# Performance work log

Measured on AMD Instinct MI355X. Metric: run time of the kernel, lower is better.

## Reference

```python
import jax, jax.numpy as jnp
import numpy as np

B, CIN, CMID, COUT, H, W = 4, 64, 128, 128, 128, 128
K = 9  # 3x3 taps
EPS = 1e-5


def conv3x3(x, w, b):
    # standard 3x3 conv, stride 1, pad 1, NCHW / OIHW
    y = jax.lax.conv_general_dilated(x, w, (1, 1), ((1, 1), (1, 1)),
                                     dimension_numbers=('NCHW', 'OIHW', 'NCHW'))
    return y + b[None, :, None, None]


def deform_conv3x3(x, offset, w, b):
    # torchvision DeformConv2d semantics (v1, no mask), kernel 3, pad 1, stride 1.
    # offset: [B, 2*K, H, W] with per-tap (dy, dx) pairs.
    Bn, C, Hn, Wn = x.shape
    off = offset.reshape(Bn, K, 2, Hn, Wn)
    off_y, off_x = off[:, :, 0], off[:, :, 1]          # [B,K,H,W]
    ky = (jnp.arange(K) // 3).astype(x.dtype)          # tap row 0..2
    kx = (jnp.arange(K) % 3).astype(x.dtype)           # tap col 0..2
    # sampling positions: p = out_pos - pad + tap + offset
    py = jnp.arange(Hn, dtype=x.dtype)[None, None, :, None] - 1.0 + ky[None, :, None, None] + off_y
    px = jnp.arange(Wn, dtype=x.dtype)[None, None, None, :] - 1.0 + kx[None, :, None, None] + off_x
    y0 = jnp.floor(py); x0 = jnp.floor(px)
    wy1 = py - y0; wx1 = px - x0                       # bilinear fractions
    y0i = y0.astype(jnp.int32); x0i = x0.astype(jnp.int32)
    xf = x.reshape(Bn, C, Hn * Wn)

    def gather(iy, ix):
        valid = ((iy >= 0) & (iy < Hn) & (ix >= 0) & (ix < Wn)).astype(x.dtype)
        idx = jnp.clip(iy, 0, Hn - 1) * Wn + jnp.clip(ix, 0, Wn - 1)  # [B,K,H,W]
        g = jax.vmap(lambda xb, ib: xb[:, ib])(xf, idx)               # [B,C,K,H,W]
        return g, valid

    g00, v00 = gather(y0i, x0i)
    g01, v01 = gather(y0i, x0i + 1)
    g10, v10 = gather(y0i + 1, x0i)
    g11, v11 = gather(y0i + 1, x0i + 1)

    def wmul(g, v, wgt):
        return g * (v * wgt)[:, None]                  # broadcast over channel dim

    sampled = (wmul(g00, v00, (1 - wy1) * (1 - wx1)) +
               wmul(g01, v01, (1 - wy1) * wx1) +
               wmul(g10, v10, wy1 * (1 - wx1)) +
               wmul(g11, v11, wy1 * wx1))              # [B,C,K,H,W]
    out = jnp.einsum('bckhw,ock->bohw', sampled, w.reshape(w.shape[0], C, K))
    return out + b[None, :, None, None]


def batchnorm_relu(x, gamma, beta):
    # training-mode BN: batch statistics over (N,H,W), biased variance
    mean = jnp.mean(x, axis=(0, 2, 3), keepdims=True)
    var = jnp.mean(jnp.square(x - mean), axis=(0, 2, 3), keepdims=True)
    y = (x - mean) * jax.lax.rsqrt(var + EPS)
    return jax.nn.relu(y * gamma[None, :, None, None] + beta[None, :, None, None])


def setup_inputs() -> dict:
    key = jax.random.key(0)
    ks = jax.random.split(key, 13)
    s = 0.05  # small weights keep offsets small / sampling mostly in-bounds
    return {
        'x': jax.random.normal(ks[0], (B, CIN, H, W), jnp.float32),
        'w_off1': jax.random.normal(ks[1], (2 * K, CIN, 3, 3), jnp.float32) * s,
        'b_off1': jnp.zeros((2 * K,), jnp.float32),
        'w1': jax.random.normal(ks[2], (CMID, CIN, 3, 3), jnp.float32) * s,
        'b1': jax.random.normal(ks[3], (CMID,), jnp.float32) * s,
        'g1': jnp.ones((CMID,), jnp.float32),
        'be1': jnp.zeros((CMID,), jnp.float32),
        'w_off2': jax.random.normal(ks[4], (2 * K, CMID, 3, 3), jnp.float32) * s,
        'b_off2': jnp.zeros((2 * K,), jnp.float32),
        'w2': jax.random.normal(ks[5], (COUT, CMID, 3, 3), jnp.float32) * s,
        'b2': jax.random.normal(ks[6], (COUT,), jnp.float32) * s,
        'g2': jnp.ones((COUT,), jnp.float32),
        'be2': jnp.zeros((COUT,), jnp.float32),
    }


def reference(x, w_off1, b_off1, w1, b1, g1, be1, w_off2, b_off2, w2, b2, g2, be2):
    offset1 = conv3x3(x, w_off1, b_off1)
    out = deform_conv3x3(x, offset1, w1, b1)
    out = batchnorm_relu(out, g1, be1)
    offset2 = conv3x3(out, w_off2, b_off2)
    out = deform_conv3x3(out, offset2, w2, b2)
    out = batchnorm_relu(out, g2, be2)
    return out
```

## Files before the change

kernel.cpp:

```cpp
#include <hip/hip_runtime.h>
#include <hip/hip_bf16.h>

#define BB 4
#define H_ 128
#define W_ 128
#define HWP 16384
#define CIN1 64
#define CMID 128
#define KOFF 18

typedef short short8 __attribute__((ext_vector_type(8)));
typedef float floatx4 __attribute__((ext_vector_type(4)));

#define WS_AB   16
#define WS_CVT  288
#define CVT_TOTAL 4447396
#define WS_WF1  4447744
#define WS_WF2  4484608
#define WS_XT   4558336
#define WS_OFF  6655488
#define WS_Y1   7835136
#define WS_Y1T  16223744
#define WS_PART 21600000
#define WS_Y2   WS_Y1

#define R_X     0
#define R_WOFF1 4194304
#define R_BOFF1 4204672
#define R_W1    4204690
#define R_B1    4278418
#define R_G1    4278546
#define R_BE1   4278674
#define R_WOFF2 4278802
#define R_BOFF2 4299538
#define R_W2    4299556
#define R_B2    4447012
#define R_G2    4447140
#define R_BE2   4447268

struct SrcPtrs { const void* p[13]; };

__device__ inline short f2bf(float f) {
    __hip_bfloat16 h = __float2bfloat16(f);
    return *reinterpret_cast<short*>(&h);
}
__device__ inline float bf2f(unsigned short u) {
    return __uint_as_float(((unsigned int)u) << 16);
}
__device__ inline float bfu_lo(unsigned int u) { return __uint_as_float(u << 16); }
__device__ inline float bfu_hi(unsigned int u) { return __uint_as_float(u & 0xFFFF0000u); }
__device__ inline float rl_f(float v, int i) {
    return __int_as_float(__builtin_amdgcn_readlane(__float_as_int(v), i));
}

__global__ void probe_dtype_k(const unsigned int* __restrict__ g1, int* __restrict__ flag) {
    if (threadIdx.x == 0 && blockIdx.x == 0) {
        flag[0] = ((g1[0] & 0xFFFFu) != 0u) ? 1 : 0;
    }
}

__global__ __launch_bounds__(256) void convert_inputs_k(SrcPtrs sp, float* __restrict__ dst,
                                                        const int* __restrict__ flag, int total) {
    int i = blockIdx.x * 256 + threadIdx.x;
    if (i >= total) return;
    constexpr int prefix[13] = {0, R_WOFF1, R_BOFF1, R_W1, R_B1, R_G1, R_BE1,
                                R_WOFF2, R_BOFF2, R_W2, R_B2, R_G2, R_BE2};
    const void* src = sp.p[0];
    int base = 0;
#pragma unroll
    for (int q = 1; q < 13; ++q) {
        if (i >= prefix[q]) { src = sp.p[q]; base = prefix[q]; }
    }
    int local = i - base;
    float v;
    if (flag[0] != 0) {
        v = bf2f(((const unsigned short*)src)[local]);
    } else {
        v = ((const float*)src)[local];
    }
    dst[i] = v;
}

template <int CIN>
__global__ __launch_bounds__(256) void wf_build_k(const float* __restrict__ w, short* __restrict__ wf) {
    constexpr int KSTEPS = CIN * 9 / 32;
    int idx = blockIdx.x * 256 + threadIdx.x;
    int j    = idx & 7;
    int lane = (idx >> 3) & 63;
    int rem  = idx >> 9;
    int ks   = rem % KSTEPS;
    int ct   = rem / KSTEPS;
    int co = ct * 16 + (lane & 15);
    int k  = ks * 32 + (lane >> 4) * 8 + j;
    int ci = k & (CIN - 1);
    int kk = k / CIN;
    wf[idx] = f2bf(w[(co * CIN + ci) * 9 + kk]);
}

__global__ __launch_bounds__(256) void xt_build_k(const float* __restrict__ x, unsigned short* __restrict__ xt) {
    __shared__ __align__(4) short s_t[64 * 66];
    int bi  = blockIdx.x;
    int hw0 = (bi & 255) * 64;
    int b   = bi >> 8;
    int t   = threadIdx.x;
    int hwp = t & 63;
#pragma unroll
    for (int it = 0; it < 16; ++it) {
        int c = it * 4 + (t >> 6);
        float v = x[((long)(b * 64 + c) << 14) + hw0 + hwp];
        s_t[hwp * 66 + c] = f2bf(v);
    }
    __syncthreads();
#pragma unroll
    for (int it = 0; it < 8; ++it) {
        int i  = it * 256 + t;
        int c2 = (i & 31) * 2;
        int hw2 = i >> 5;
        int sv = *(const int*)&s_t[hw2 * 66 + c2];
        *(int*)&xt[((long)((b << 14) + hw0 + hw2)) * 64 + c2] = sv;
    }
}

template <int CIN>
__global__ __launch_bounds__(256) void conv3x3_atomic_k(const float* __restrict__ x,
                                                        const float* __restrict__ w,
                                                        const float* __restrict__ bias,
                                                        float* __restrict__ outp) {
    constexpr int CIQ = CIN / 4;
    int bi = blockIdx.x;
    int h  = bi & 127;
    int b  = (bi >> 7) & 3;
    int q  = bi >> 9;
    int t  = threadIdx.x;
    int wq = t & 127;
    int cg = __builtin_amdgcn_readfirstlane(t >> 7);
    int co0 = cg * 9;
    int ci0 = q * CIQ;

    float acc[9];
#pragma unroll
    for (int j = 0; j < 9; ++j) acc[j] = (q == 0) ? bias[co0 + j] : 0.f;

    const float* xb = x + ((long)(b * CIN + ci0) << 14);
    bool bm = h > 0, bp = h < H_ - 1, bl = wq > 0, br = wq < W_ - 1;
    int rm = (bm ? h - 1 : 0) << 7;
    int rc = h << 7;
    int rp = (bp ? h + 1 : H_ - 1) << 7;

#pragma unroll 2
    for (int ci = 0; ci < CIQ; ++ci) {
        const float* plane = xb + ((long)ci << 14);
        float v0 = plane[rm + wq - 1], v1 = plane[rm + wq], v2 = plane[rm + wq + 1];
        float v3 = plane[rc + wq - 1], v4 = plane[rc + wq], v5 = plane[rc + wq + 1];
        float v6 = plane[rp + wq - 1], v7 = plane[rp + wq], v8 = plane[rp + wq + 1];
        v0 = (bm && bl) ? v0 : 0.f;
        v1 = bm ? v1 : 0.f;
        v2 = (bm && br) ? v2 : 0.f;
        v3 = bl ? v3 : 0.f;
        v5 = br ? v5 : 0.f;
        v6 = (bp && bl) ? v6 : 0.f;
        v7 = bp ? v7 : 0.f;
        v8 = (bp && br) ? v8 : 0.f;
#pragma unroll
        for (int j = 0; j < 9; ++j) {
            const float* wk = w + ((long)(co0 + j) * CIN + ci0 + ci) * 9;
            acc[j] += v0 * wk[0] + v1 * wk[1] + v2 * wk[2]
                    + v3 * wk[3] + v4 * wk[4] + v5 * wk[5]
                    + v6 * wk[6] + v7 * wk[7] + v8 * wk[8];
        }
    }

    long ob = ((long)(b * KOFF + co0) << 14) + (h << 7) + wq;
#pragma unroll
    for (int j = 0; j < 9; ++j) atomicAdd(&outp[ob + ((long)j << 14)], acc[j]);
}

template <int CIN>
__device__ inline void build_table(const float* __restrict__ off, int b, int h, int w0,
                                   int lane, int wv,
                                   int& tpk, float& tw0, float& tw1, float& tw2, float& tw3) {
    tpk = 0; tw0 = tw1 = tw2 = tw3 = 0.f;
    if (lane < 36) {
        int r = wv + 4 * lane;
        int p = r & 15;
        int k = r >> 4;
        int wpix = w0 + p;
        long obase = ((long)(b * KOFF) << 14) + (h << 7) + wpix;
        float oy = off[obase + ((long)(2 * k) << 14)];
        float ox = off[obase + ((long)(2 * k + 1) << 14)];
        float py = (float)(h - 1 + (k / 3)) + oy;
        float px = (float)(wpix - 1 + (k % 3)) + ox;
        float fy = floorf(py), fx = floorf(px);
        float wy = py - fy, wx = px - fx;
        int y0 = (int)fy, x0 = (int)fx;
        int y1 = y0 + 1, x1 = x0 + 1;
        bool vy0 = (y0 >= 0) && (y0 < H_);
        bool vy1 = (y1 >= 0) && (y1 < H_);
        bool vx0 = (x0 >= 0) && (x0 < W_);
        bool vx1 = (x1 >= 0) && (x1 < W_);
        float wy0 = 1.f - wy, wx0 = 1.f - wx;
        tw0 = (vy0 && vx0) ? wy0 * wx0 : 0.f;
        tw1 = (vy0 && vx1) ? wy0 * wx  : 0.f;
        tw2 = (vy1 && vx0) ? wy  * wx0 : 0.f;
        tw3 = (vy1 && vx1) ? wy  * wx  : 0.f;
        int iy0 = min(max(y0, 0), H_ - 1), iy1 = min(max(y1, 0), H_ - 1);
        int ix0 = min(max(x0, 0), W_ - 1), ix1 = min(max(x1, 0), W_ - 1);
        int dx = ix1 - ix0;
        int dy = iy1 - iy0;
        tpk = (iy0 * W_ + ix0) | (dx << 14) | (dy << 15);
    }
}

template <int NB>
__device__ inline void gather_batch128(const unsigned short* __restrict__ xb, short* __restrict__ s_samp,
                                       int PADc, int i0, int kkbase, int wv, int lane,
                                       int tpk, float tw0, float tw1, float tw2, float tw3) {
    uint4 ub[NB];
#pragma unroll
    for (int j = 0; j < NB; ++j) {
        int pk = __builtin_amdgcn_readlane(tpk, i0 + j);
        const unsigned short* b00 = xb + (pk & 0x3FFF) * 128;
        const unsigned short* b01 = b00 + ((pk >> 14) & 1) * 128;
        const unsigned short* b10 = b00 + ((pk >> 15) & 1) * (W_ * 128);
        const unsigned short* b11 = b01 + ((pk >> 15) & 1) * (W_ * 128);
        ub[j].x = *(const unsigned int*)(b00 + 2 * lane);
        ub[j].y = *(const unsigned int*)(b01 + 2 * lane);
        ub[j].z = *(const unsigned int*)(b10 + 2 * lane);
        ub[j].w = *(const unsigned int*)(b11 + 2 * lane);
    }
#pragma unroll
    for (int j = 0; j < NB; ++j) {
        int i = i0 + j;
        int r = wv + 4 * i;
        float w00 = rl_f(tw0, i), w01 = rl_f(tw1, i), w10 = rl_f(tw2, i), w11 = rl_f(tw3, i);
        float vlo = w00 * bfu_lo(ub[j].x) + w01 * bfu_lo(ub[j].y)
                  + w10 * bfu_lo(ub[j].z) + w11 * bfu_lo(ub[j].w);
        float vhi = w00 * bfu_hi(ub[j].x) + w01 * bfu_hi(ub[j].y)
                  + w10 * bfu_hi(ub[j].z) + w11 * bfu_hi(ub[j].w);
        __hip_bfloat162 h2 = __float22bfloat162_rn(make_float2(vlo, vhi));
        *(unsigned int*)&s_samp[(r & 15) * PADc + ((r >> 4) - kkbase) * 128 + 2 * lane] =
            *reinterpret_cast<unsigned int*>(&h2);
    }
}

template <int NB>
__device__ inline void gather_batch64(const unsigned short* __restrict__ xb, short* __restrict__ s_samp,
                                      int PADc, int i0, int wv, int lane,
                                      int tpk, float tw0, float tw1, float tw2, float tw3) {
    unsigned short q0[NB], q1[NB], q2[NB], q3[NB];
#pragma unroll
    for (int j = 0; j < NB; ++j) {
        int pk = __builtin_amdgcn_readlane(tpk, i0 + j);
        const unsigned short* b00 = xb + (pk & 0x3FFF) * 64;
        const unsigned short* b01 = b00 + ((pk >> 14) & 1) * 64;
        const unsigned short* b10 = b00 + ((pk >> 15) & 1) * (W_ * 64);
        const unsigned short* b11 = b01 + ((pk >> 15) & 1) * (W_ * 64);
        q0[j] = b00[lane]; q1[j] = b01[lane]; q2[j] = b10[lane]; q3[j] = b11[lane];
    }
#pragma unroll
    for (int j = 0; j < NB; ++j) {
        int i = i0 + j;
        int r = wv + 4 * i;
        float w00 = rl_f(tw0, i), w01 = rl_f(tw1, i), w10 = rl_f(tw2, i), w11 = rl_f(tw3, i);
        float v = w00 * bf2f(q0[j]) + w01 * bf2f(q1[j]) + w10 * bf2f(q2[j]) + w11 * bf2f(q3[j]);
        s_samp[(r & 15) * PADc + (r >> 4) * 64 + lane] = f2bf(v);
    }
}

__global__ __launch_bounds__(256, 5) void deform_mfma64_k(const unsigned short* __restrict__ xt,
                                                          const float* __restrict__ off,
                                                          const short* __restrict__ wf,
                                                          const float* __restrict__ bias,
                                                          float* __restrict__ out) {
    constexpr int CIN = 64;
    constexpr int K = 576;
    constexpr int PADc = K + 8;
    constexpr int KSTEPS = K / 32;
    __shared__ __align__(16) short s_samp[16 * PADc];

    int bi = blockIdx.x;
    int w0 = (bi & 7) * 16;
    int h  = (bi >> 3) & 127;
    int b  = bi >> 10;
    int t  = threadIdx.x;
    int lane = t & 63;
    int wv   = t >> 6;

    int tpk; float tw0, tw1, tw2, tw3;
    build_table<CIN>(off, b, h, w0, lane, wv, tpk, tw0, tw1, tw2, tw3);
    const unsigned short* xb = xt + (long)b * HWP * CIN;

    gather_batch64<12>(xb, s_samp, PADc,  0, wv, lane, tpk, tw0, tw1, tw2, tw3);
    gather_batch64<12>(xb, s_samp, PADc, 12, wv, lane, tpk, tw0, tw1, tw2, tw3);
    gather_batch64<12>(xb, s_samp, PADc, 24, wv, lane, tpk, tw0, tw1, tw2, tw3);
    __syncthreads();

    int p_   = lane & 15;
    int quad = lane >> 4;
    int ct0 = wv * 2, ct1 = wv * 2 + 1;
    floatx4 acc0, acc1;
#pragma unroll
    for (int r = 0; r < 4; ++r) {
        acc0[r] = bias[ct0 * 16 + quad * 4 + r];
        acc1[r] = bias[ct1 * 16 + quad * 4 + r];
    }
#pragma unroll 3
    for (int ks = 0; ks < KSTEPS; ++ks) {
        short8 bfrag = *(const short8*)&s_samp[p_ * PADc + ks * 32 + quad * 8];
        short8 a0 = *(const short8*)&wf[(((long)ct0 * KSTEPS + ks) * 64 + lane) * 8];
        short8 a1 = *(const short8*)&wf[(((long)ct1 * KSTEPS + ks) * 64 + lane) * 8];
        acc0 = __builtin_amdgcn_mfma_f32_16x16x32_bf16(a0, bfrag, acc0, 0, 0, 0);
        acc1 = __builtin_amdgcn_mfma_f32_16x16x32_bf16(a1, bfrag, acc1, 0, 0, 0);
    }

    long ob = ((long)(b * 128) << 14) + (h << 7) + w0 + p_;
#pragma unroll
    for (int r = 0; r < 4; ++r) {
        out[ob + ((long)(ct0 * 16 + quad * 4 + r) << 14)] = acc0[r];
        out[ob + ((long)(ct1 * 16 + quad * 4 + r) << 14)] = acc1[r];
    }
}

__global__ __launch_bounds__(256, 5) void deform_mfma128_k(const unsigned short* __restrict__ xt,
                                                           const float* __restrict__ off,
                                                           const short* __restrict__ wf,
                                                           const float* __restrict__ bias,
                                                           float* __restrict__ out) {
    constexpr int KSTEPS = 36;
    constexpr int PADc = 5 * 128 + 8;
    __shared__ __align__(16) short s_samp[16 * PADc];

    int bi = blockIdx.x;
    int w0 = (bi & 7) * 16;
    int h  = (bi >> 3) & 127;
    int b  = bi >> 10;
    int t  = threadIdx.x;
    int lane = t & 63;
    int wv   = t >> 6;

    int tpk; float tw0, tw1, tw2, tw3;
    build_table<128>(off, b, h, w0, lane, wv, tpk, tw0, tw1, tw2, tw3);
    const unsigned short* xb = xt + (long)b * HWP * 128;

    int p_   = lane & 15;
    int quad = lane >> 4;
    int ct0 = wv * 2, ct1 = wv * 2 + 1;
    floatx4 acc0, acc1;
#pragma unroll
    for (int r = 0; r < 4; ++r) {
        acc0[r] = bias[ct0 * 16 + quad * 4 + r];
        acc1[r] = bias[ct1 * 16 + quad * 4 + r];
    }

    gather_batch128<8>(xb, s_samp, PADc, 0, 0, wv, lane, tpk, tw0, tw1, tw2, tw3);
    gather_batch128<8>(xb, s_samp, PADc, 8, 0, wv, lane, tpk, tw0, tw1, tw2, tw3);
    __syncthreads();
#pragma unroll 4
    for (int ks = 0; ks < 16; ++ks) {
        short8 bfrag = *(const short8*)&s_samp[p_ * PADc + ks * 32 + quad * 8];
        short8 a0 = *(const short8*)&wf[(((long)ct0 * KSTEPS + ks) * 64 + lane) * 8];
        short8 a1 = *(const short8*)&wf[(((long)ct1 * KSTEPS + ks) * 64 + lane) * 8];
        acc0 = __builtin_amdgcn_mfma_f32_16x16x32_bf16(a0, bfrag, acc0, 0, 0, 0);
        acc1 = __builtin_amdgcn_mfma_f32_16x16x32_bf16(a1, bfrag, acc1, 0, 0, 0);
    }
    __syncthreads();

    gather_batch128<10>(xb, s_samp, PADc, 16, 4, wv, lane, tpk, tw0, tw1, tw2, tw3);
    gather_batch128<10>(xb, s_samp, PADc, 26, 4, wv, lane, tpk, tw0, tw1, tw2, tw3);
    __syncthreads();
#pragma unroll 4
    for (int ks = 16; ks < 36; ++ks) {
        short8 bfrag = *(const short8*)&s_samp[p_ * PADc + (ks - 16) * 32 + quad * 8];
        short8 a0 = *(const short8*)&wf[(((long)ct0 * KSTEPS + ks) * 64 + lane) * 8];
        short8 a1 = *(const short8*)&wf[(((long)ct1 * KSTEPS + ks) * 64 + lane) * 8];
        acc0 = __builtin_amdgcn_mfma_f32_16x16x32_bf16(a0, bfrag, acc0, 0, 0, 0);
        acc1 = __builtin_amdgcn_mfma_f32_16x16x32_bf16(a1, bfrag, acc1, 0, 0, 0);
    }

    long ob = ((long)(b * 128) << 14) + (h << 7) + w0 + p_;
#pragma unroll
    for (int r = 0; r < 4; ++r) {
        out[ob + ((long)(ct0 * 16 + quad * 4 + r) << 14)] = acc0[r];
        out[ob + ((long)(ct1 * 16 + quad * 4 + r) << 14)] = acc1[r];
    }
}

__global__ __launch_bounds__(256) void bn_stats_part_k(const float* __restrict__ y, float* __restrict__ part) {
    int bi = blockIdx.x;
    int c = bi & 127;
    int b = bi >> 7;
    int t = threadIdx.x;
    const float4* p4 = (const float4*)(y + ((long)(b * 128 + c) << 14));
    float sum = 0.f, ss = 0.f;
#pragma unroll
    for (int i = 0; i < 16; ++i) {
        float4 v = p4[t + 256 * i];
        sum += v.x + v.y + v.z + v.w;
        ss  += v.x * v.x + v.y * v.y + v.z * v.z + v.w * v.w;
    }
#pragma unroll
    for (int o = 32; o > 0; o >>= 1) { sum += __shfl_down(sum, o); ss += __shfl_down(ss, o); }
    __shared__ float s1[4], s2[4];
    int wave = t >> 6;
    if ((t & 63) == 0) { s1[wave] = sum; s2[wave] = ss; }
    __syncthreads();
    if (t == 0) {
        part[bi]       = s1[0] + s1[1] + s1[2] + s1[3];
        part[512 + bi] = s2[0] + s2[1] + s2[2] + s2[3];
    }
}

__global__ void bn_final_k(const float* __restrict__ part, const float* __restrict__ g,
                           const float* __restrict__ be, float* __restrict__ ab) {
    int c = threadIdx.x;
    float sum = 0.f, ss = 0.f;
#pragma unroll
    for (int b = 0; b < 4; ++b) {
        sum += part[b * 128 + c];
        ss  += part[512 + b * 128 + c];
    }
    float mean = sum * (1.f / 65536.f);
    float var  = ss  * (1.f / 65536.f) - mean * mean;
    float inv  = rsqrtf(var + 1e-5f);
    float a = g[c] * inv;
    ab[c]       = a;
    ab[128 + c] = be[c] - mean * a;
}

__global__ __launch_bounds__(256) void bn_apply_dual_k(float* __restrict__ y, const float* __restrict__ ab,
                                                       unsigned short* __restrict__ yt) {
    __shared__ __align__(4) short s_t[64 * 134];
    int bi  = blockIdx.x;
    int hw0 = (bi & 255) * 64;
    int b   = bi >> 8;
    int t   = threadIdx.x;
    int hwp = t & 63;
#pragma unroll 4
    for (int it = 0; it < 32; ++it) {
        int c = it * 4 + (t >> 6);
        float a = ab[c], sh = ab[128 + c];
        long addr = ((long)(b * 128 + c) << 14) + hw0 + hwp;
        float v = y[addr];
        v = fmaxf(v * a + sh, 0.f);
        y[addr] = v;
        s_t[hwp * 134 + c] = f2bf(v);
    }
    __syncthreads();
#pragma unroll 4
    for (int it = 0; it < 16; ++it) {
        int i   = it * 256 + t;
        int c2  = (i & 63) * 2;
        int hw2 = i >> 6;
        int sv = *(const int*)&s_t[hw2 * 134 + c2];
        *(int*)&yt[((long)((b << 14) + hw0 + hw2)) * 128 + c2] = sv;
    }
}

__global__ __launch_bounds__(256) void bn_apply_out_k(const float* __restrict__ y, const float* __restrict__ ab,
                                                      const int* __restrict__ flag, void* __restrict__ out, int total4) {
    int i = blockIdx.x * 256 + threadIdx.x;
    if (i >= total4) return;
    int c = (i >> 12) & 127;
    float a = ab[c], sh = ab[128 + c];
    float4 v = reinterpret_cast<const float4*>(y)[i];
    v.x = fmaxf(v.x * a + sh, 0.f);
    v.y = fmaxf(v.y * a + sh, 0.f);
    v.z = fmaxf(v.z * a + sh, 0.f);
    v.w = fmaxf(v.w * a + sh, 0.f);
    if (flag[0] != 0) {
        ushort4 u;
        u.x = (unsigned short)f2bf(v.x);
        u.y = (unsigned short)f2bf(v.y);
        u.z = (unsigned short)f2bf(v.z);
        u.w = (unsigned short)f2bf(v.w);
        reinterpret_cast<ushort4*>(out)[i] = u;
    } else {
        reinterpret_cast<float4*>(out)[i] = v;
    }
}

extern "C" void kernel_launch(void* const* d_in, const int* in_sizes, int n_in,
                              void* d_out, int out_size, void* d_ws, size_t ws_size,
                              hipStream_t stream) {
    float* ws   = (float*)d_ws;
    int*   flag = (int*)d_ws;
    float* ab   = ws + WS_AB;
    float* cvt  = ws + WS_CVT;

    const float* X     = cvt + R_X;
    const float* Woff1 = cvt + R_WOFF1;
    const float* Boff1 = cvt + R_BOFF1;
    const float* W1f   = cvt + R_W1;
    const float* B1f   = cvt + R_B1;
    const float* G1    = cvt + R_G1;
    const float* Be1   = cvt + R_BE1;
    const float* Woff2 = cvt + R_WOFF2;
    const float* Boff2 = cvt + R_BOFF2;
    const float* W2f   = cvt + R_W2;
    const float* B2f   = cvt + R_B2;
    const float* G2    = cvt + R_G2;
    const float* Be2   = cvt + R_BE2;

    short* WF1 = (short*)(ws + WS_WF1);
    short* WF2 = (short*)(ws + WS_WF2);
    unsigned short* XT  = (unsigned short*)(ws + WS_XT);
    unsigned short* Y1T = (unsigned short*)(ws + WS_Y1T);
    float* OFF  = ws + WS_OFF;
    float* PART = ws + WS_PART;
    float* Y1   = ws + WS_Y1;
    float* Y2   = ws + WS_Y2;

    SrcPtrs sp;
    for (int j = 0; j < 13; ++j) sp.p[j] = d_in[j];

    probe_dtype_k<<<1, 64, 0, stream>>>((const unsigned int*)d_in[5], flag);
    convert_inputs_k<<<(CVT_TOTAL + 255) / 256, 256, 0, stream>>>(sp, cvt, flag, CVT_TOTAL);
    wf_build_k<64><<<288, 256, 0, stream>>>(W1f, WF1);
    wf_build_k<128><<<576, 256, 0, stream>>>(W2f, WF2);
    xt_build_k<<<1024, 256, 0, stream>>>(X, XT);

    hipMemsetAsync(OFF, 0, (size_t)KOFF * 65536 * 4, stream);
    conv3x3_atomic_k<64><<<BB * 128 * 4, 256, 0, stream>>>(X, Woff1, Boff1, OFF);
    deform_mfma64_k<<<BB * 128 * 8, 256, 0, stream>>>(XT, OFF, WF1, B1f, Y1);
    bn_stats_part_k<<<512, 256, 0, stream>>>(Y1, PART);
    bn_final_k<<<1, 128, 0, stream>>>(PART, G1, Be1, ab);
    bn_apply_dual_k<<<1024, 256, 0, stream>>>(Y1, ab, Y1T);

    hipMemsetAsync(OFF, 0, (size_t)KOFF * 65536 * 4, stream);
    conv3x3_atomic_k<128><<<BB * 128 * 4, 256, 0, stream>>>(Y1, Woff2, Boff2, OFF);
    deform_mfma128_k<<<BB * 128 * 8, 256, 0, stream>>>(Y1T, OFF, WF2, B2f, Y2);
    bn_stats_part_k<<<512, 256, 0, stream>>>(Y2, PART);
    bn_final_k<<<1, 128, 0, stream>>>(PART, G2, Be2, ab);
    bn_apply_out_k<<<(BB * 128 * HWP / 4 + 255) / 256, 256, 0, stream>>>(Y2, ab, flag, d_out, BB * 128 * HWP / 4);
}
```

Before: 358.8 us.

## Give each wave its own 16-pixel tile with all output channels and per-tap streaming

Both deformable-conv kernels now assign each wave an independent 16-pixel strip and compute all 128 output channels (8 MFMA accumulators), instead of splitting output channels across waves that share one gathered tile. Sampling and MFMA are interleaved per tap in a small per-wave LDS slice, removing block-wide __syncthreads and shrinking shared memory. Blocks cover 64 pixels, so the grid is four times smaller. The trade is more accumulator registers and lower occupancy (launch bound 4). Each wave also loads the full weight fragment set, which costs more weight traffic per pixel, in exchange for reusing each gathered sample across all channels.

```diff
diff --git a/kernel.cpp b/kernel.cpp
--- a/kernel.cpp
+++ b/kernel.cpp
@@ -175,214 +175,194 @@
     for (int j = 0; j < 9; ++j) atomicAdd(&outp[ob + ((long)j << 14)], acc[j]);
 }
 
-template <int CIN>
-__device__ inline void build_table(const float* __restrict__ off, int b, int h, int w0,
-                                   int lane, int wv,
-                                   int& tpk, float& tw0, float& tw1, float& tw2, float& tw3) {
-    tpk = 0; tw0 = tw1 = tw2 = tw3 = 0.f;
-    if (lane < 36) {
-        int r = wv + 4 * lane;
-        int p = r & 15;
-        int k = r >> 4;
-        int wpix = w0 + p;
-        long obase = ((long)(b * KOFF) << 14) + (h << 7) + wpix;
-        float oy = off[obase + ((long)(2 * k) << 14)];
-        float ox = off[obase + ((long)(2 * k + 1) << 14)];
-        float py = (float)(h - 1 + (k / 3)) + oy;
-        float px = (float)(wpix - 1 + (k % 3)) + ox;
-        float fy = floorf(py), fx = floorf(px);
-        float wy = py - fy, wx = px - fx;
-        int y0 = (int)fy, x0 = (int)fx;
-        int y1 = y0 + 1, x1 = x0 + 1;
-        bool vy0 = (y0 >= 0) && (y0 < H_);
-        bool vy1 = (y1 >= 0) && (y1 < H_);
-        bool vx0 = (x0 >= 0) && (x0 < W_);
-        bool vx1 = (x1 >= 0) && (x1 < W_);
-        float wy0 = 1.f - wy, wx0 = 1.f - wx;
-        tw0 = (vy0 && vx0) ? wy0 * wx0 : 0.f;
-        tw1 = (vy0 && vx1) ? wy0 * wx  : 0.f;
-        tw2 = (vy1 && vx0) ? wy  * wx0 : 0.f;
-        tw3 = (vy1 && vx1) ? wy  * wx  : 0.f;
-        int iy0 = min(max(y0, 0), H_ - 1), iy1 = min(max(y1, 0), H_ - 1);
-        int ix0 = min(max(x0, 0), W_ - 1), ix1 = min(max(x1, 0), W_ - 1);
-        int dx = ix1 - ix0;
-        int dy = iy1 - iy0;
-        tpk = (iy0 * W_ + ix0) | (dx << 14) | (dy << 15);
-    }
-}
-
-template <int NB>
-__device__ inline void gather_batch128(const unsigned short* __restrict__ xb, short* __restrict__ s_samp,
-                                       int PADc, int i0, int kkbase, int wv, int lane,
-                                       int tpk, float tw0, float tw1, float tw2, float tw3) {
-    uint4 ub[NB];
-#pragma unroll
-    for (int j = 0; j < NB; ++j) {
-        int pk = __builtin_amdgcn_readlane(tpk, i0 + j);
-        const unsigned short* b00 = xb + (pk & 0x3FFF) * 128;
-        const unsigned short* b01 = b00 + ((pk >> 14) & 1) * 128;
-        const unsigned short* b10 = b00 + ((pk >> 15) & 1) * (W_ * 128);
-        const unsigned short* b11 = b01 + ((pk >> 15) & 1) * (W_ * 128);
-        ub[j].x = *(const unsigned int*)(b00 + 2 * lane);
-        ub[j].y = *(const unsigned int*)(b01 + 2 * lane);
-        ub[j].z = *(const unsigned int*)(b10 + 2 * lane);
-        ub[j].w = *(const unsigned int*)(b11 + 2 * lane);
-    }
-#pragma unroll
-    for (int j = 0; j < NB; ++j) {
-        int i = i0 + j;
-        int r = wv + 4 * i;
-        float w00 = rl_f(tw0, i), w01 = rl_f(tw1, i), w10 = rl_f(tw2, i), w11 = rl_f(tw3, i);
-        float vlo = w00 * bfu_lo(ub[j].x) + w01 * bfu_lo(ub[j].y)
-                  + w10 * bfu_lo(ub[j].z) + w11 * bfu_lo(ub[j].w);
-        float vhi = w00 * bfu_hi(ub[j].x) + w01 * bfu_hi(ub[j].y)
-                  + w10 * bfu_hi(ub[j].z) + w11 * bfu_hi(ub[j].w);
-        __hip_bfloat162 h2 = __float22bfloat162_rn(make_float2(vlo, vhi));
-        *(unsigned int*)&s_samp[(r & 15) * PADc + ((r >> 4) - kkbase) * 128 + 2 * lane] =
-            *reinterpret_cast<unsigned int*>(&h2);
-    }
-}
-
-template <int NB>
-__device__ inline void gather_batch64(const unsigned short* __restrict__ xb, short* __restrict__ s_samp,
-                                      int PADc, int i0, int wv, int lane,
-                                      int tpk, float tw0, float tw1, float tw2, float tw3) {
-    unsigned short q0[NB], q1[NB], q2[NB], q3[NB];
-#pragma unroll
-    for (int j = 0; j < NB; ++j) {
-        int pk = __builtin_amdgcn_readlane(tpk, i0 + j);
-        const unsigned short* b00 = xb + (pk & 0x3FFF) * 64;
-        const unsigned short* b01 = b00 + ((pk >> 14) & 1) * 64;
-        const unsigned short* b10 = b00 + ((pk >> 15) & 1) * (W_ * 64);
-        const unsigned short* b11 = b01 + ((pk >> 15) & 1) * (W_ * 64);
-        q0[j] = b00[lane]; q1[j] = b01[lane]; q2[j] = b10[lane]; q3[j] = b11[lane];
-    }
-#pragma unroll
-    for (int j = 0; j < NB; ++j) {
-        int i = i0 + j;
-        int r = wv + 4 * i;
-        float w00 = rl_f(tw0, i), w01 = rl_f(tw1, i), w10 = rl_f(tw2, i), w11 = rl_f(tw3, i);
-        float v = w00 * bf2f(q0[j]) + w01 * bf2f(q1[j]) + w10 * bf2f(q2[j]) + w11 * bf2f(q3[j]);
-        s_samp[(r & 15) * PADc + (r >> 4) * 64 + lane] = f2bf(v);
-    }
-}
-
-__global__ __launch_bounds__(256, 5) void deform_mfma64_k(const unsigned short* __restrict__ xt,
+__device__ inline void build_table3(const float* __restrict__ off, int b, int h, int wpx0, int lane,
+                                    int (&tpk)[3], float (&t0)[3], float (&t1)[3],
+                                    float (&t2)[3], float (&t3)[3]) {
+#pragma unroll
+    for (int s = 0; s < 3; ++s) {
+        tpk[s] = 0; t0[s] = t1[s] = t2[s] = t3[s] = 0.f;
+        int kk = s * 4 + (lane >> 4);
+        int p  = lane & 15;
+        if (kk < 9) {
+            int wpix = wpx0 + p;
+            long obase = ((long)(b * KOFF) << 14) + (h << 7) + wpix;
+            float oy = off[obase + ((long)(2 * kk) << 14)];
+            float ox = off[obase + ((long)(2 * kk + 1) << 14)];
+            float py = (float)(h - 1 + (kk / 3)) + oy;
+            float px = (float)(wpix - 1 + (kk % 3)) + ox;
+            float fy = floorf(py), fx = floorf(px);
+            float wy = py - fy, wx = px - fx;
+            int y0 = (int)fy, x0 = (int)fx;
+            int y1 = y0 + 1, x1 = x0 + 1;
+            bool vy0 = (y0 >= 0) && (y0 < H_);
+            bool vy1 = (y1 >= 0) && (y1 < H_);
+            bool vx0 = (x0 >= 0) && (x0 < W_);
+            bool vx1 = (x1 >= 0) && (x1 < W_);
+            float wy0 = 1.f - wy, wx0 = 1.f - wx;
+            t0[s] = (vy0 && vx0) ? wy0 * wx0 : 0.f;
+            t1[s] = (vy0 && vx1) ? wy0 * wx  : 0.f;
+            t2[s] = (vy1 && vx0) ? wy  * wx0 : 0.f;
+            t3[s] = (vy1 && vx1) ? wy  * wx  : 0.f;
+            int iy0 = min(max(y0, 0), H_ - 1), iy1 = min(max(y1, 0), H_ - 1);
+            int ix0 = min(max(x0, 0), W_ - 1), ix1 = min(max(x1, 0), W_ - 1);
+            tpk[s] = (iy0 * W_ + ix0) | ((ix1 - ix0) << 14) | ((iy1 - iy0) << 15);
+        }
+    }
+}
+
+__global__ __launch_bounds__(256, 4) void deform_mfma128_k(const unsigned short* __restrict__ xt,
+                                                           const float* __restrict__ off,
+                                                           const short* __restrict__ wf,
+                                                           const float* __restrict__ bias,
+                                                           float* __restrict__ out) {
+    constexpr int PADR = 136;
+    __shared__ __align__(16) short s_samp[64 * PADR];
+
+    int bi  = blockIdx.x;
+    int w0b = (bi & 1) * 64;
+    int h   = (bi >> 1) & 127;
+    int b   = bi >> 8;
+    int t = threadIdx.x;
+    int lane = t & 63, wv = t >> 6;
+    int wpx0 = w0b + wv * 16;
+
+    int tpk[3]; float t0[3], t1[3], t2[3], t3[3];
+    build_table3(off, b, h, wpx0, lane, tpk, t0, t1, t2, t3);
+
+    const unsigned short* xb = xt + (long)b * HWP * 128;
+    short* sw = s_samp + wv * 16 * PADR;
+    int p_ = lane & 15, quad = lane >> 4;
+
+    floatx4 acc[8];
+#pragma unroll
+    for (int ct = 0; ct < 8; ++ct)
+#pragma unroll
+        for (int r = 0; r < 4; ++r) acc[ct][r] = bias[ct * 16 + quad * 4 + r];
+
+#pragma unroll
+    for (int c = 0; c < 9; ++c) {
+        int s = c >> 2;
+#pragma unroll
+        for (int pb = 0; pb < 4; ++pb) {
+            uint4 u[4]; float a0[4], a1[4], a2[4], a3[4];
+#pragma unroll
+            for (int j = 0; j < 4; ++j) {
+                int li = ((c & 3) << 4) | (pb * 4 + j);
+                int pk = __builtin_amdgcn_readlane(tpk[s], li);
+                a0[j] = rl_f(t0[s], li); a1[j] = rl_f(t1[s], li);
+                a2[j] = rl_f(t2[s], li); a3[j] = rl_f(t3[s], li);
+                const unsigned short* b00 = xb + (pk & 0x3FFF) * 128;
+                const unsigned short* b01 = b00 + ((pk >> 14) & 1) * 128;
+                const unsigned short* b10 = b00 + ((pk >> 15) & 1) * (W_ * 128);
+                const unsigned short* b11 = b01 + ((pk >> 15) & 1) * (W_ * 128);
+                u[j].x = *(const unsigned int*)(b00 + 2 * lane);
+                u[j].y = *(const unsigned int*)(b01 + 2 * lane);
+                u[j].z = *(const unsigned int*)(b10 + 2 * lane);
+                u[j].w = *(const unsigned int*)(b11 + 2 * lane);
+            }
+#pragma unroll
+            for (int j = 0; j < 4; ++j) {
+                float vlo = a0[j] * bfu_lo(u[j].x) + a1[j] * bfu_lo(u[j].y)
+                          + a2[j] * bfu_lo(u[j].z) + a3[j] * bfu_lo(u[j].w);
+                float vhi = a0[j] * bfu_hi(u[j].x) + a1[j] * bfu_hi(u[j].y)
+                          + a2[j] * bfu_hi(u[j].z) + a3[j] * bfu_hi(u[j].w);
+                __hip_bfloat162 h2 = __float22bfloat162_rn(make_float2(vlo, vhi));
+                *(unsigned int*)&sw[(pb * 4 + j) * PADR + 2 * lane] = *reinterpret_cast<unsigned int*>(&h2);
+            }
+        }
+#pragma unroll
+        for (int ksl = 0; ksl < 4; ++ksl) {
+            int ks = c * 4 + ksl;
+            short8 bfrag = *(const short8*)&sw[p_ * PADR + ksl * 32 + quad * 8];
+#pragma unroll
+            for (int ct = 0; ct < 8; ++ct) {
+                short8 a = *(const short8*)&wf[(((long)ct * 36 + ks) * 64 + lane) * 8];
+                acc[ct] = __builtin_amdgcn_mfma_f32_16x16x32_bf16(a, bfrag, acc[ct], 0, 0, 0);
+            }
+        }
+    }
+
+    long ob = ((long)(b * 128) << 14) + (h << 7) + wpx0 + p_;
+#pragma unroll
+    for (int ct = 0; ct < 8; ++ct)
+#pragma unroll
+        for (int r = 0; r < 4; ++r)
+            out[ob + ((long)(ct * 16 + quad * 4 + r) << 14)] = acc[ct][r];
+}
+
+__global__ __launch_bounds__(256, 4) void deform_mfma64_k(const unsigned short* __restrict__ xt,
                                                           const float* __restrict__ off,
                                                           const short* __restrict__ wf,
                                                           const float* __restrict__ bias,
                                                           float* __restrict__ out) {
-    constexpr int CIN = 64;
-    constexpr int K = 576;
-    constexpr int PADc = K + 8;
-    constexpr int KSTEPS = K / 32;
-    __shared__ __align__(16) short s_samp[16 * PADc];
-
-    int bi = blockIdx.x;
-    int w0 = (bi & 7) * 16;
-    int h  = (bi >> 3) & 127;
-    int b  = bi >> 10;
-    int t  = threadIdx.x;
-    int lane = t & 63;
-    int wv   = t >> 6;
-
-    int tpk; float tw0, tw1, tw2, tw3;
-    build_table<CIN>(off, b, h, w0, lane, wv, tpk, tw0, tw1, tw2, tw3);
-    const unsigned short* xb = xt + (long)b * HWP * CIN;
-
-    gather_batch64<12>(xb, s_samp, PADc,  0, wv, lane, tpk, tw0, tw1, tw2, tw3);
-    gather_batch64<12>(xb, s_samp, PADc, 12, wv, lane, tpk, tw0, tw1, tw2, tw3);
-    gather_batch64<12>(xb, s_samp, PADc, 24, wv, lane, tpk, tw0, tw1, tw2, tw3);
-    __syncthreads();
-
-    int p_   = lane & 15;
-    int quad = lane >> 4;
-    int ct0 = wv * 2, ct1 = wv * 2 + 1;
-    floatx4 acc0, acc1;
-#pragma unroll
-    for (int r = 0; r < 4; ++r) {
-        acc0[r] = bias[ct0 * 16 + quad * 4 + r];
-        acc1[r] = bias[ct1 * 16 + quad * 4 + r];
-    }
-#pragma unroll 3
-    for (int ks = 0; ks < KSTEPS; ++ks) {
-        short8 bfrag = *(const short8*)&s_samp[p_ * PADc + ks * 32 + quad * 8];
-        short8 a0 = *(const short8*)&wf[(((long)ct0 * KSTEPS + ks) * 64 + lane) * 8];
-        short8 a1 = *(const short8*)&wf[(((long)ct1 * KSTEPS + ks) * 64 + lane) * 8];
-        acc0 = __builtin_amdgcn_mfma_f32_16x16x32_bf16(a0, bfrag, acc0, 0, 0, 0);
-        acc1 = __builtin_amdgcn_mfma_f32_16x16x32_bf16(a1, bfrag, acc1, 0, 0, 0);
-    }
-
-    long ob = ((long)(b * 128) << 14) + (h << 7) + w0 + p_;
-#pragma unroll
-    for (int r = 0; r < 4; ++r) {
-        out[ob + ((long)(ct0 * 16 + quad * 4 + r) << 14)] = acc0[r];
-        out[ob + ((long)(ct1 * 16 + quad * 4 + r) << 14)] = acc1[r];
-    }
-}
-
-__global__ __launch_bounds__(256, 5) void deform_mfma128_k(const unsigned short* __restrict__ xt,
-                                                           const float* __restrict__ off,
-                                                           const short* __restrict__ wf,
-                                                           const float* __restrict__ bias,
-                                                           float* __restrict__ out) {
-    constexpr int KSTEPS = 36;
-    constexpr int PADc = 5 * 128 + 8;
-    __shared__ __align__(16) short s_samp[16 * PADc];
-
-    int bi = blockIdx.x;
-    int w0 = (bi & 7) * 16;
-    int h  = (bi >> 3) & 127;
-    int b  = bi >> 10;
-    int t  = threadIdx.x;
-    int lane = t & 63;
-    int wv   = t >> 6;
-
-    int tpk; float tw0, tw1, tw2, tw3;
-    build_table<128>(off, b, h, w0, lane, wv, tpk, tw0, tw1, tw2, tw3);
-    const unsigned short* xb = xt + (long)b * HWP * 128;
-
-    int p_   = lane & 15;
-    int quad = lane >> 4;
-    int ct0 = wv * 2, ct1 = wv * 2 + 1;
-    floatx4 acc0, acc1;
-#pragma unroll
-    for (int r = 0; r < 4; ++r) {
-        acc0[r] = bias[ct0 * 16 + quad * 4 + r];
-        acc1[r] = bias[ct1 * 16 + quad * 4 + r];
-    }
-
-    gather_batch128<8>(xb, s_samp, PADc, 0, 0, wv, lane, tpk, tw0, tw1, tw2, tw3);
-    gather_batch128<8>(xb, s_samp, PADc, 8, 0, wv, lane, tpk, tw0, tw1, tw2, tw3);
-    __syncthreads();
-#pragma unroll 4
-    for (int ks = 0; ks < 16; ++ks) {
-        short8 bfrag = *(const short8*)&s_samp[p_ * PADc + ks * 32 + quad * 8];
-        short8 a0 = *(const short8*)&wf[(((long)ct0 * KSTEPS + ks) * 64 + lane) * 8];
-        short8 a1 = *(const short8*)&wf[(((long)ct1 * KSTEPS + ks) * 64 + lane) * 8];
-        acc0 = __builtin_amdgcn_mfma_f32_16x16x32_bf16(a0, bfrag, acc0, 0, 0, 0);
-        acc1 = __builtin_amdgcn_mfma_f32_16x16x32_bf16(a1, bfrag, acc1, 0, 0, 0);
-    }
-    __syncthreads();
-
-    gather_batch128<10>(xb, s_samp, PADc, 16, 4, wv, lane, tpk, tw0, tw1, tw2, tw3);
-    gather_batch128<10>(xb, s_samp, PADc, 26, 4, wv, lane, tpk, tw0, tw1, tw2, tw3);
-    __syncthreads();
-#pragma unroll 4
-    for (int ks = 16; ks < 36; ++ks) {
-        short8 bfrag = *(const short8*)&s_samp[p_ * PADc + (ks - 16) * 32 + quad * 8];
-        short8 a0 = *(const short8*)&wf[(((long)ct0 * KSTEPS + ks) * 64 + lane) * 8];
-        short8 a1 = *(const short8*)&wf[(((long)ct1 * KSTEPS + ks) * 64 + lane) * 8];
-        acc0 = __builtin_amdgcn_mfma_f32_16x16x32_bf16(a0, bfrag, acc0, 0, 0, 0);
-        acc1 = __builtin_amdgcn_mfma_f32_16x16x32_bf16(a1, bfrag, acc1, 0, 0, 0);
-    }
-
-    long ob = ((long)(b * 128) << 14) + (h << 7) + w0 + p_;
-#pragma unroll
-    for (int r = 0; r < 4; ++r) {
-        out[ob + ((long)(ct0 * 16 + quad * 4 + r) << 14)] = acc0[r];
-        out[ob + ((long)(ct1 * 16 + quad * 4 + r) << 14)] = acc1[r];
-    }
+    constexpr int PADR = 72;
+    __shared__ __align__(16) short s_samp[64 * PADR];
+
+    int bi  = blockIdx.x;
+    int w0b = (bi & 1) * 64;
+    int h   = (bi >> 1) & 127;
+    int b   = bi >> 8;
+    int t = threadIdx.x;
+    int lane = t & 63, wv = t >> 6;
+    int wpx0 = w0b + wv * 16;
+
+    int tpk[3]; float t0[3], t1[3], t2[3], t3[3];
+    build_table3(off, b, h, wpx0, lane, tpk, t0, t1, t2, t3);
+
+    const unsigned short* xb = xt + (long)b * HWP * 64;
+    short* sw = s_samp + wv * 16 * PADR;
+    int p_ = lane & 15, quad = lane >> 4;
+
+    floatx4 acc[8];
+#pragma unroll
+    for (int ct = 0; ct < 8; ++ct)
+#pragma unroll
+        for (int r = 0; r < 4; ++r) acc[ct][r] = bias[ct * 16 + quad * 4 + r];
+
+#pragma unroll
+    for (int c = 0; c < 9; ++c) {
+        int s = c >> 2;
+#pragma unroll
+        for (int pb = 0; pb < 4; ++pb) {
+            unsigned short q0[4], q1[4], q2[4], q3[4];
+            float a0[4], a1[4], a2[4], a3[4];
+#pragma unroll
+            for (int j = 0; j < 4; ++j) {
+                int li = ((c & 3) << 4) | (pb * 4 + j);
+                int pk = __builtin_amdgcn_readlane(tpk[s], li);
+                a0[j] = rl_f(t0[s], li); a1[j] = rl_f(t1[s], li);
+                a2[j] = rl_f(t2[s], li); a3[j] = rl_f(t3[s], li);
+                const unsigned short* b00 = xb + (pk & 0x3FFF) * 64;
+                const unsigned short* b01 = b00 + ((pk >> 14) & 1) * 64;
+                const unsigned short* b10 = b00 + ((pk >> 15) & 1) * (W_ * 64);
+                const unsigned short* b11 = b01 + ((pk >> 15) & 1) * (W_ * 64);
+                q0[j] = b00[lane]; q1[j] = b01[lane]; q2[j] = b10[lane]; q3[j] = b11[lane];
+            }
+#pragma unroll
+            for (int j = 0; j < 4; ++j) {
+                float v = a0[j] * bf2f(q0[j]) + a1[j] * bf2f(q1[j])
+                        + a2[j] * bf2f(q2[j]) + a3[j] * bf2f(q3[j]);
+                sw[(pb * 4 + j) * PADR + lane] = f2bf(v);
+            }
+        }
+#pragma unroll
+        for (int ksl = 0; ksl < 2; ++ksl) {
+            int ks = c * 2 + ksl;
+            short8 bfrag = *(const short8*)&sw[p_ * PADR + ksl * 32 + quad * 8];
+#pragma unroll
+            for (int ct = 0; ct < 8; ++ct) {
+                short8 a = *(const short8*)&wf[(((long)ct * 18 + ks) * 64 + lane) * 8];
+                acc[ct] = __builtin_amdgcn_mfma_f32_16x16x32_bf16(a, bfrag, acc[ct], 0, 0, 0);
+            }
+        }
+    }
+
+    long ob = ((long)(b * 128) << 14) + (h << 7) + wpx0 + p_;
+#pragma unroll
+    for (int ct = 0; ct < 8; ++ct)
+#pragma unroll
+        for (int r = 0; r < 4; ++r)
+            out[ob + ((long)(ct * 16 + quad * 4 + r) << 14)] = acc[ct][r];
 }
 
 __global__ __launch_bounds__(256) void bn_stats_part_k(const float* __restrict__ y, float* __restrict__ part) {
@@ -521,14 +501,14 @@
 
     hipMemsetAsync(OFF, 0, (size_t)KOFF * 65536 * 4, stream);
     conv3x3_atomic_k<64><<<BB * 128 * 4, 256, 0, stream>>>(X, Woff1, Boff1, OFF);
-    deform_mfma64_k<<<BB * 128 * 8, 256, 0, stream>>>(XT, OFF, WF1, B1f, Y1);
+    deform_mfma64_k<<<BB * 128 * 2, 256, 0, stream>>>(XT, OFF, WF1, B1f, Y1);
     bn_stats_part_k<<<512, 256, 0, stream>>>(Y1, PART);
     bn_final_k<<<1, 128, 0, stream>>>(PART, G1, Be1, ab);
     bn_apply_dual_k<<<1024, 256, 0, stream>>>(Y1, ab, Y1T);
 
     hipMemsetAsync(OFF, 0, (size_t)KOFF * 65536 * 4, stream);
     conv3x3_atomic_k<128><<<BB * 128 * 4, 256, 0, stream>>>(Y1, Woff2, Boff2, OFF);
-    deform_mfma128_k<<<BB * 128 * 8, 256, 0, stream>>>(Y1T, OFF, WF2, B2f, Y2);
+    deform_mfma128_k<<<BB * 128 * 2, 256, 0, stream>>>(Y1T, OFF, WF2, B2f, Y2);
     bn_stats_part_k<<<512, 256, 0, stream>>>(Y2, PART);
     bn_final_k<<<1, 128, 0, stream>>>(PART, G2, Be2, ab);
     bn_apply_out_k<<<(BB * 128 * HWP / 4 + 255) / 256, 256, 0, stream>>>(Y2, ab, flag, d_out, BB * 128 * HWP / 4);
```

New measurement: 416.5 us. 1.16x slower.
